# Optimization experiments

Hardware: AMD Instinct MI355X
Metric: run time of the kernel (lower is better)

Reference implementation:

```python
import jax, jax.numpy as jnp
import numpy as np

N_HEADS = 32
N_KV_HEADS = 8
HEAD_DIM = 64


def _apply_rope(x, cos, sin):
    # x: [b, s, h, d]; cos/sin: [s, d//2]; interleaved real/imag pairs
    xr = x[..., 0::2]
    xi = x[..., 1::2]
    c = cos[None, :, None, :]
    s = sin[None, :, None, :]
    out_r = xr * c - xi * s
    out_i = xr * s + xi * c
    return jnp.stack([out_r, out_i], axis=-1).reshape(x.shape)


def setup_inputs() -> dict:
    key = jax.random.key(0)
    ks = jax.random.split(key, 10)
    b, s, dim = 2, 512, 2048
    cache_len = 1536
    half = HEAD_DIM // 2
    pos = jnp.arange(cache_len, cache_len + s, dtype=jnp.float32)
    inv_freq = 1.0 / (10000.0 ** (jnp.arange(0, half, dtype=jnp.float32) / half))
    ang = pos[:, None] * inv_freq[None, :]
    scale = 0.02
    return {
        "x": jax.random.normal(ks[0], (b, s, dim), jnp.float32),
        "freqs_cos": jnp.cos(ang),
        "freqs_sin": jnp.sin(ang),
        "k_cache": jax.random.normal(ks[1], (b, N_KV_HEADS, cache_len, HEAD_DIM), jnp.float32),
        "v_cache": jax.random.normal(ks[2], (b, N_KV_HEADS, cache_len, HEAD_DIM), jnp.float32),
        "attn_mask": jnp.zeros((s, cache_len + s), jnp.float32),
        "wq": jax.random.normal(ks[3], (N_HEADS * HEAD_DIM, dim), jnp.float32) * scale,
        "wk": jax.random.normal(ks[4], (N_KV_HEADS * HEAD_DIM, dim), jnp.float32) * scale,
        "wv": jax.random.normal(ks[5], (N_KV_HEADS * HEAD_DIM, dim), jnp.float32) * scale,
        "wo": jax.random.normal(ks[6], (dim, N_HEADS * HEAD_DIM), jnp.float32) * scale,
    }


def reference(x, freqs_cos, freqs_sin, k_cache, v_cache, attn_mask, wq, wk, wv, wo):
    b, s, dim = x.shape
    n_rep = N_HEADS // N_KV_HEADS
    # QKV projections (nn.Linear: y = x @ W.T)
    q = (x @ wq.T).reshape(b, s, N_HEADS, HEAD_DIM)
    k = (x @ wk.T).reshape(b, s, N_KV_HEADS, HEAD_DIM)
    v = (x @ wv.T).reshape(b, s, N_KV_HEADS, HEAD_DIM)
    # RoPE on q, k
    q = _apply_rope(q, freqs_cos, freqs_sin)
    k = _apply_rope(k, freqs_cos, freqs_sin)
    # [b, h, s, d]
    q = q.transpose(0, 2, 1, 3)
    k = k.transpose(0, 2, 1, 3)
    v = v.transpose(0, 2, 1, 3)
    new_k, new_v = k, v
    # KV-cache concat along sequence dim
    k_full = jnp.concatenate([k_cache, k], axis=2)
    v_full = jnp.concatenate([v_cache, v], axis=2)
    # GQA: repeat_interleave kv heads
    if n_rep > 1:
        k_full = jnp.repeat(k_full, n_rep, axis=1)
        v_full = jnp.repeat(v_full, n_rep, axis=1)
    # SDPA
    scale = 1.0 / jnp.sqrt(jnp.asarray(HEAD_DIM, x.dtype))
    scores = jnp.einsum("bhqd,bhkd->bhqk", q, k_full) * scale + attn_mask
    probs = jax.nn.softmax(scores, axis=-1)
    out = jnp.einsum("bhqk,bhkd->bhqd", probs, v_full)
    out = out.transpose(0, 2, 1, 3).reshape(b, s, N_HEADS * HEAD_DIM)
    out = out @ wo.T
    return (out, new_k, new_v)
```

## Files before the change

### kernel.cpp

```cpp
#include <hip/hip_runtime.h>
#include <hip/hip_bf16.h>

typedef __attribute__((ext_vector_type(8))) short bf16x8;
typedef __attribute__((ext_vector_type(4))) float f32x4;
typedef unsigned short u16;

#define MFMA16(a, b, c) __builtin_amdgcn_mfma_f32_16x16x32_bf16(a, b, c, 0, 0, 0)
#define GLL(srcp, dstp) __builtin_amdgcn_global_load_lds(                      \
    (const __attribute__((address_space(1))) void*)(srcp),                     \
    (__attribute__((address_space(3))) void*)(dstp), 16, 0, 0)

__device__ __forceinline__ u16 f2b(float f) {
  union { float f; unsigned u; } a; a.f = f;
  return (u16)((a.u + 0x7FFFu + ((a.u >> 16) & 1u)) >> 16);
}
__device__ __forceinline__ unsigned pk2(float lo, float hi) {
  __hip_bfloat162 h = __float22bfloat162_rn(make_float2(lo, hi));
  return *reinterpret_cast<unsigned*>(&h);
}

__global__ __launch_bounds__(256) void prep(const float* __restrict__ x,
                                            const float* __restrict__ kc,
                                            u16* __restrict__ xb,
                                            u16* __restrict__ kfull) {
  const int c = blockIdx.x * 256 + threadIdx.x;
  const float* src;
  u16* dst;
  if (c < 524288) {
    src = x + (size_t)c * 4; dst = xb + (size_t)c * 4;
  } else {
    int l = c - 524288;
    int bh = l / 24576, r = l - bh * 24576;
    src = kc + (size_t)bh * 98304 + (size_t)r * 4;
    dst = kfull + (size_t)bh * 131072 + (size_t)r * 4;
  }
  const float4 v = *(const float4*)src;
  ushort4 o;
  o.x = f2b(v.x); o.y = f2b(v.y); o.z = f2b(v.z); o.w = f2b(v.w);
  *(ushort4*)dst = o;
}

__global__ __launch_bounds__(256) void vtr(const float* __restrict__ vc,
                                           const float* __restrict__ newv,
                                           u16* __restrict__ vT) {
  __shared__ float tile[64][65];
  const int kt = blockIdx.x, bh = blockIdx.y;
  const float* src;
  int colbase;
  if (kt < 24) {
    src = vc + ((size_t)bh * 1536 + (size_t)kt * 64) * 64;
    colbase = kt * 64;
  } else {
    src = newv + ((size_t)bh * 512 + (size_t)(kt - 24) * 64) * 64;
    colbase = 1536 + (kt - 24) * 64;
  }
  const int t = threadIdx.x;
#pragma unroll
  for (int j = 0; j < 4; j++) {
    int e = t + j * 256;
    int r = e >> 4, c = (e & 15) * 4;
    float4 v = *(const float4*)(src + (size_t)r * 64 + c);
    tile[r][c] = v.x; tile[r][c + 1] = v.y; tile[r][c + 2] = v.z; tile[r][c + 3] = v.w;
  }
  __syncthreads();
  int d = t >> 2, kv0 = (t & 3) * 16;
  u16* dst = vT + ((size_t)bh * 64 + d) * 2048 + colbase + kv0;
#pragma unroll
  for (int i = 0; i < 16; i++) dst[i] = f2b(tile[kv0 + i][d]);
}

__global__ __launch_bounds__(256, 3) void gemm_bt(const u16* __restrict__ A,
                                                  const float* __restrict__ B0,
                                                  const float* __restrict__ B1,
                                                  const float* __restrict__ B2,
                                                  float* __restrict__ Cp,
                                                  int M, int N, int K, int nb1, int nb2) {
  __shared__ __attribute__((aligned(16))) u16 As[2][4096];
  __shared__ __attribute__((aligned(16))) u16 Bs[2][8192];
  const int t = threadIdx.x;
  const int lane = t & 63, w = t >> 6;
  const int wr = (w >> 1) * 32, wc = (w & 1) * 64;
  const int g = lane >> 4, cc = lane & 15;
  const int nby = N >> 7, cpx = nby >> 3, nrt = M >> 6;
  const int j = blockIdx.x & 7, q = blockIdx.x >> 3;
  const int ct = j * cpx + (q % cpx);
  const int rest = q / cpx;
  const int rt = rest % nrt, ks = rest / nrt;
  const size_t row0 = (size_t)rt * 64;
  const int col0 = ct * 128;
  const int k0base = ks * (K >> 1);

  const int lr = lane >> 3, lc = lane & 7;
  const int swz = lc ^ lr;
  const u16* aS = A + (row0 + w * 16 + lr) * (size_t)K + swz * 8 + k0base;
  const float* Bb;
  int brow;
  if (col0 < nb1) { Bb = B0; brow = col0; }
  else if (col0 < nb2) { Bb = B1; brow = col0 - nb1; }
  else { Bb = B2; brow = col0 - nb2; }
  const float* bS = Bb + (brow + w * 32 + lr) * (size_t)K + swz * 8 + k0base;

  f32x4 acc[2][4] = {};
  f32x4 bl[4][2];

#define ALOAD(bufi, kk0)                                                       \
  {                                                                            \
    _Pragma("unroll") for (int i = 0; i < 2; i++)                              \
        GLL(aS + (size_t)(i * 8) * K + (kk0), &As[bufi][(w * 16 + i * 8) * 64]); \
  }
#define BLOAD(kk0)                                                             \
  {                                                                            \
    _Pragma("unroll") for (int i = 0; i < 4; i++) {                            \
      bl[i][0] = *(const f32x4*)(bS + (size_t)(i * 8) * K + (kk0));            \
      bl[i][1] = *(const f32x4*)(bS + (size_t)(i * 8) * K + (kk0) + 4);        \
    }                                                                          \
  }
#define BWRITE(bufi)                                                           \
  {                                                                            \
    _Pragma("unroll") for (int i = 0; i < 4; i++) {                            \
      uint4 pw;                                                                \
      pw.x = pk2(bl[i][0][0], bl[i][0][1]);                                    \
      pw.y = pk2(bl[i][0][2], bl[i][0][3]);                                    \
      pw.z = pk2(bl[i][1][0], bl[i][1][1]);                                    \
      pw.w = pk2(bl[i][1][2], bl[i][1][3]);                                    \
      *(uint4*)&Bs[bufi][(w * 32 + i * 8 + lr) * 64 + lc * 8] = pw;            \
    }                                                                          \
  }

  const int niter = (K >> 1) >> 6;
  BLOAD(0);
  ALOAD(0, 0);
  BWRITE(0);
  __syncthreads();

  for (int it = 0; it < niter; ++it) {
    const int buf = it & 1;
    if (it + 1 < niter) {
      BLOAD((it + 1) * 64);
      ALOAD(buf ^ 1, (it + 1) * 64);
    }
    bf16x8 av[2][2], bv[4][2];
#pragma unroll
    for (int m = 0; m < 2; m++) {
      const int row = wr + m * 16 + cc;
#pragma unroll
      for (int kk = 0; kk < 2; kk++)
        av[m][kk] = *(const bf16x8*)(&As[buf][row * 64 + (((kk * 4 + g) ^ (cc & 7)) * 8)]);
    }
#pragma unroll
    for (int n = 0; n < 4; n++) {
      const int row = wc + n * 16 + cc;
#pragma unroll
      for (int kk = 0; kk < 2; kk++)
        bv[n][kk] = *(const bf16x8*)(&Bs[buf][row * 64 + (((kk * 4 + g) ^ (cc & 7)) * 8)]);
    }
#pragma unroll
    for (int kk = 0; kk < 2; kk++)
#pragma unroll
      for (int m = 0; m < 2; m++)
#pragma unroll
        for (int n = 0; n < 4; n++)
          acc[m][n] = MFMA16(av[m][kk], bv[n][kk], acc[m][n]);
    if (it + 1 < niter) BWRITE(buf ^ 1);
    __syncthreads();
  }
#undef ALOAD
#undef BLOAD
#undef BWRITE
  float* Cw = Cp + (size_t)ks * M * N;
#pragma unroll
  for (int m = 0; m < 2; m++)
#pragma unroll
    for (int n = 0; n < 4; n++)
#pragma unroll
      for (int r = 0; r < 4; r++)
        Cw[(row0 + wr + m * 16 + g * 4 + r) * N + (col0 + wc + n * 16 + cc)] = acc[m][n][r];
}

__global__ __launch_bounds__(256) void postproc(const float* __restrict__ Cp0,
                                                const float* __restrict__ Cp1,
                                                const float* __restrict__ fcos,
                                                const float* __restrict__ fsin,
                                                u16* __restrict__ qrope,
                                                u16* __restrict__ kfull,
                                                float* __restrict__ newk,
                                                float* __restrict__ newv) {
  int idx = blockIdx.x * 256 + threadIdx.x;
  if (idx >= 1024 * 1536) return;
  int m = idx / 1536, p = idx - m * 1536;
  int b = m >> 9, s = m & 511;
  const float* r0 = Cp0 + (size_t)m * 3072;
  const float* r1 = Cp1 + (size_t)m * 3072;
  if (p < 1280) {
    bool isq = p < 1024;
    int pk = isq ? p : p - 1024;
    int h = pk >> 5, i = pk & 31;
    int colbase = (isq ? 0 : 2048) + h * 64 + 2 * i;
    float xr = r0[colbase] + r1[colbase];
    float xi = r0[colbase + 1] + r1[colbase + 1];
    float co = fcos[s * 32 + i], si = fsin[s * 32 + i];
    float orr = xr * co - xi * si;
    float oii = xr * si + xi * co;
    if (isq) {
      u16* dst = qrope + (((size_t)(b * 32 + h) * 512 + s) * 64 + 2 * i);
      dst[0] = f2b(orr); dst[1] = f2b(oii);
    } else {
      size_t o0 = ((size_t)(b * 8 + h) * 512 + s) * 64 + 2 * i;
      newk[o0] = orr; newk[o0 + 1] = oii;
      u16* kf = kfull + (((size_t)(b * 8 + h) * 2048 + 1536 + s) * 64 + 2 * i);
      kf[0] = f2b(orr); kf[1] = f2b(oii);
    }
  } else {
    int pv = p - 1280;
    int h = pv >> 5, i = pv & 31;
    int cb = 2560 + h * 64 + 2 * i;
    float v0 = r0[cb] + r1[cb], v1 = r0[cb + 1] + r1[cb + 1];
    size_t o0 = ((size_t)(b * 8 + h) * 512 + s) * 64 + 2 * i;
    newv[o0] = v0; newv[o0 + 1] = v1;
  }
}

__global__ __launch_bounds__(256) void sumout(const float* __restrict__ a,
                                              const float* __restrict__ b,
                                              float* __restrict__ out) {
  const int i = blockIdx.x * 256 + threadIdx.x;
  const float4 va = *(const float4*)(a + (size_t)i * 4);
  const float4 vb = *(const float4*)(b + (size_t)i * 4);
  float4 o;
  o.x = va.x + vb.x; o.y = va.y + vb.y; o.z = va.z + vb.z; o.w = va.w + vb.w;
  *(float4*)(out + (size_t)i * 4) = o;
}

__global__ __launch_bounds__(512, 4) void attn_split(const u16* __restrict__ qrope,
                                                     const u16* __restrict__ kfull,
                                                     const u16* __restrict__ vT,
                                                     const float* __restrict__ mask,
                                                     float* __restrict__ po,
                                                     float* __restrict__ ml) {
  __shared__ __attribute__((aligned(16))) u16 Ks[4][4096];
  __shared__ __attribute__((aligned(16))) u16 Vs[4][4096];
  __shared__ __attribute__((aligned(16))) u16 P_lds[8192];
  const int t = threadIdx.x, lane = t & 63, w = t >> 6;
  const int g = lane >> 4, cc = lane & 15;
  const int p = blockIdx.x;
  const int v = (p & 7) * 64 + (p >> 3);
  const int bh = v >> 3, qt = (v >> 1) & 3, sp = v & 1;
  const int b = bh >> 5, h = bh & 31;
  const int bhkv = b * 8 + (h >> 2);
  const int s0 = qt * 128 + w * 16;
  const int j0beg = sp * 1024;

  const int lr = lane >> 3, lc = lane & 7;
  const int swzc = lc ^ lr;

  bf16x8 qa0, qa1;
  {
    const u16* qb = qrope + ((size_t)bh * 512 + s0 + cc) * 64 + g * 8;
    qa0 = *(const bf16x8*)qb;
    qa1 = *(const bf16x8*)(qb + 32);
  }
  float mrow[4], lsum[4];
  f32x4 o[4] = {};
#pragma unroll
  for (int r = 0; r < 4; r++) { mrow[r] = -1e30f; lsum[r] = 0.0f; }

  u16* Pw = P_lds + w * 1024;
  const float* mbase = mask + (size_t)(s0 + g * 4) * 2048 + cc;
  const u16* ksrc0 = kfull + (size_t)bhkv * 131072 + (size_t)(w * 8 + lr) * 64 + swzc * 8;
  const u16* vsrc0 = vT + ((size_t)bhkv * 64 + w * 8 + lr) * 2048 + swzc * 8;

#pragma unroll
  for (int pt = 0; pt < 3; ++pt) {
    GLL(ksrc0 + (size_t)(j0beg + pt * 64) * 64, &Ks[pt][w * 512]);
    GLL(vsrc0 + (j0beg + pt * 64), &Vs[pt][w * 512]);
  }

  for (int it = 0; it < 16; ++it) {
    const int buf = it & 3;
    const int j0 = j0beg + it * 64;
    if (it < 14) {
      asm volatile("s_waitcnt vmcnt(4)" ::: "memory");
    } else if (it == 14) {
      asm volatile("s_waitcnt vmcnt(2)" ::: "memory");
    } else {
      asm volatile("s_waitcnt vmcnt(0)" ::: "memory");
    }
    __builtin_amdgcn_s_barrier();

    float mk[4][4];
#pragma unroll
    for (int r = 0; r < 4; r++)
#pragma unroll
      for (int jb = 0; jb < 4; jb++)
        mk[r][jb] = mbase[(size_t)r * 2048 + j0 + jb * 16];
    __builtin_amdgcn_sched_barrier(0);
    if (it < 13) {
      GLL(ksrc0 + (size_t)(j0 + 192) * 64, &Ks[(it + 3) & 3][w * 512]);
      GLL(vsrc0 + (j0 + 192), &Vs[(it + 3) & 3][w * 512]);
    }

    f32x4 sc[4];
    __builtin_amdgcn_s_setprio(1);
#pragma unroll
    for (int jb = 0; jb < 4; jb++) {
      const bf16x8 k0 = *(const bf16x8*)(&Ks[buf][(jb * 16 + cc) * 64 + ((g ^ (cc & 7)) * 8)]);
      const bf16x8 k1 =
          *(const bf16x8*)(&Ks[buf][(jb * 16 + cc) * 64 + (((g + 4) ^ (cc & 7)) * 8)]);
      f32x4 z = {0.f, 0.f, 0.f, 0.f};
      z = MFMA16(qa0, k0, z);
      z = MFMA16(qa1, k1, z);
      sc[jb] = z;
    }
    __builtin_amdgcn_s_setprio(0);
    float pp[4][4];
#pragma unroll
    for (int r = 0; r < 4; r++) {
#pragma unroll
      for (int jb = 0; jb < 4; jb++)
        pp[r][jb] = sc[jb][r] * 0.125f + mk[r][jb];
      const float lm = fmaxf(fmaxf(pp[r][0], pp[r][1]), fmaxf(pp[r][2], pp[r][3]));
      if (__any(lm > mrow[r] + 8.0f)) {
        float tm = lm;
#pragma unroll
        for (int off = 1; off < 16; off <<= 1) tm = fmaxf(tm, __shfl_xor(tm, off, 64));
        const float newm = fmaxf(mrow[r], tm);
        const float corr = __expf(mrow[r] - newm);
        mrow[r] = newm;
        lsum[r] *= corr;
#pragma unroll
        for (int db = 0; db < 4; db++) o[db][r] *= corr;
      }
      float ps = 0.f;
#pragma unroll
      for (int jb = 0; jb < 4; jb++) { pp[r][jb] = __expf(pp[r][jb] - mrow[r]); ps += pp[r][jb]; }
      lsum[r] += ps;
      const int rowb = (g * 4 + r) * 128;
      const int sw = ((g * 4 + r) & 7) << 4;
#pragma unroll
      for (int jb = 0; jb < 4; jb++)
        Pw[((rowb + (jb * 16 + cc) * 2) ^ sw) >> 1] = f2b(pp[r][jb]);
    }
    __builtin_amdgcn_s_setprio(1);
#pragma unroll
    for (int kk = 0; kk < 2; kk++) {
      const bf16x8 pa =
          *(const bf16x8*)(Pw + (((cc * 128 + kk * 64 + g * 16) ^ ((cc & 7) << 4)) >> 1));
#pragma unroll
      for (int db = 0; db < 4; db++) {
        const bf16x8 vf =
            *(const bf16x8*)(&Vs[buf][(db * 16 + cc) * 64 + (((kk * 4 + g) ^ (cc & 7)) * 8)]);
        o[db] = MFMA16(pa, vf, o[db]);
      }
    }
    __builtin_amdgcn_s_setprio(0);
  }
#pragma unroll
  for (int r = 0; r < 4; r++) {
    float ps = lsum[r];
#pragma unroll
    for (int off = 1; off < 16; off <<= 1) ps += __shfl_xor(ps, off, 64);
    const size_t row = (size_t)bh * 512 + s0 + g * 4 + r;
    float* dst = po + (row * 2 + sp) * 64 + cc;
#pragma unroll
    for (int db = 0; db < 4; db++) dst[db * 16] = o[db][r];
    if (cc == 0) {
      float2* mlp = (float2*)ml;
      mlp[row * 2 + sp] = make_float2(mrow[r], ps);
    }
  }
}

__global__ __launch_bounds__(256) void attn_combine(const float* __restrict__ po,
                                                    const float* __restrict__ ml,
                                                    u16* __restrict__ aout) {
  const int t = threadIdx.x;
  const int row = blockIdx.x * 4 + (t >> 6);
  const int d = t & 63;
  const int bh = row >> 9, s = row & 511;
  const int b = bh >> 5, h = bh & 31;
  const float2* mlp = (const float2*)ml;
  const float2 m0 = mlp[row * 2 + 0], m1 = mlp[row * 2 + 1];
  const float M = fmaxf(m0.x, m1.x);
  const float w0 = __expf(m0.x - M), w1 = __expf(m1.x - M);
  const float L = m0.y * w0 + m1.y * w1;
  const float o = po[(size_t)(row * 2 + 0) * 64 + d] * w0 +
                  po[(size_t)(row * 2 + 1) * 64 + d] * w1;
  aout[((size_t)(b * 512 + s)) * 2048 + h * 64 + d] = f2b(o / L);
}

extern "C" void kernel_launch(void* const* d_in, const int* in_sizes, int n_in,
                              void* d_out, int out_size, void* d_ws, size_t ws_size,
                              hipStream_t stream) {
  (void)in_sizes; (void)n_in; (void)out_size; (void)ws_size;
  const float* x    = (const float*)d_in[0];
  const float* fcos = (const float*)d_in[1];
  const float* fsin = (const float*)d_in[2];
  const float* kc   = (const float*)d_in[3];
  const float* vc   = (const float*)d_in[4];
  const float* mask = (const float*)d_in[5];
  const float* wq   = (const float*)d_in[6];
  const float* wk   = (const float*)d_in[7];
  const float* wv   = (const float*)d_in[8];
  const float* wo   = (const float*)d_in[9];

  float* out_f = (float*)d_out;
  float* newk  = out_f + 2097152;
  float* newv  = out_f + 2621440;

  u16*   xb    = (u16*)d_ws;
  float* Cp    = (float*)(xb + 2097152);
  float* Cp1   = Cp + 3145728;
  u16*   qrope = (u16*)(Cp + 6291456);
  u16*   kfull = qrope + 2097152;
  u16*   vTf   = kfull + 2097152;
  u16*   aout  = vTf + 2097152;
  float* ml    = (float*)(aout + 2097152);
  float* po    = (float*)d_ws;
  float* Co    = (float*)d_ws;
  float* Co1   = Co + 2097152;

  prep<<<3584, 256, 0, stream>>>(x, kc, xb, kfull);

  gemm_bt<<<768, 256, 0, stream>>>(xb, wq, wk, wv, Cp,
                                   1024, 3072, 2048, 2048, 2560);
  postproc<<<6144, 256, 0, stream>>>(Cp, Cp1, fcos, fsin, qrope, kfull, newk, newv);
  vtr<<<dim3(32, 16), 256, 0, stream>>>(vc, newv, vTf);
  attn_split<<<512, 512, 0, stream>>>(qrope, kfull, vTf, mask, po, ml);
  attn_combine<<<8192, 256, 0, stream>>>(po, ml, aout);
  gemm_bt<<<512, 256, 0, stream>>>(aout, wo, wo, wo, Co,
                                   1024, 2048, 2048, 4096, 8192);
  sumout<<<2048, 256, 0, stream>>>(Co, Co1, out_f);
}
```

Measured before the change: 124.5 us.

## Prefetch B tiles two iterations ahead with manual waitcnt barriers in GEMM

Restructures the split-K GEMM main loop so the fp32 B tile is loaded two iterations ahead into alternating register sets, while A keeps its one-ahead global_load_lds double buffering. The loop is unrolled by two, and __syncthreads is replaced by explicit s_waitcnt vmcnt/lgkmcnt plus s_barrier, so outstanding B loads can stay in flight across the barrier. The goal is to hide global load latency for B behind more MFMA work. In exchange it uses more VGPRs, which may lower occupancy. The hand-tuned vmcnt count also assumes a fixed number of loads and that niter is even.

Result: no change. 124.2 us (-0.2%).

```diff
diff --git a/kernel.cpp b/kernel.cpp
--- a/kernel.cpp
+++ b/kernel.cpp
@@ -101,72 +101,84 @@
   const float* bS = Bb + (brow + w * 32 + lr) * (size_t)K + swz * 8 + k0base;
 
   f32x4 acc[2][4] = {};
-  f32x4 bl[4][2];
+  f32x4 blA[4][2], blB[4][2];
 
 #define ALOAD(bufi, kk0)                                                       \
   {                                                                            \
     _Pragma("unroll") for (int i = 0; i < 2; i++)                              \
         GLL(aS + (size_t)(i * 8) * K + (kk0), &As[bufi][(w * 16 + i * 8) * 64]); \
   }
-#define BLOAD(kk0)                                                             \
+#define BLOAD(blv, kk0)                                                        \
   {                                                                            \
     _Pragma("unroll") for (int i = 0; i < 4; i++) {                            \
-      bl[i][0] = *(const f32x4*)(bS + (size_t)(i * 8) * K + (kk0));            \
-      bl[i][1] = *(const f32x4*)(bS + (size_t)(i * 8) * K + (kk0) + 4);        \
+      blv[i][0] = *(const f32x4*)(bS + (size_t)(i * 8) * K + (kk0));           \
+      blv[i][1] = *(const f32x4*)(bS + (size_t)(i * 8) * K + (kk0) + 4);       \
     }                                                                          \
   }
-#define BWRITE(bufi)                                                           \
+#define BWRITE(blv, bufi)                                                      \
   {                                                                            \
     _Pragma("unroll") for (int i = 0; i < 4; i++) {                            \
       uint4 pw;                                                                \
-      pw.x = pk2(bl[i][0][0], bl[i][0][1]);                                    \
-      pw.y = pk2(bl[i][0][2], bl[i][0][3]);                                    \
-      pw.z = pk2(bl[i][1][0], bl[i][1][1]);                                    \
-      pw.w = pk2(bl[i][1][2], bl[i][1][3]);                                    \
+      pw.x = pk2(blv[i][0][0], blv[i][0][1]);                                  \
+      pw.y = pk2(blv[i][0][2], blv[i][0][3]);                                  \
+      pw.z = pk2(blv[i][1][0], blv[i][1][1]);                                  \
+      pw.w = pk2(blv[i][1][2], blv[i][1][3]);                                  \
       *(uint4*)&Bs[bufi][(w * 32 + i * 8 + lr) * 64 + lc * 8] = pw;            \
     }                                                                          \
   }
 
   const int niter = (K >> 1) >> 6;
-  BLOAD(0);
+
   ALOAD(0, 0);
-  BWRITE(0);
-  __syncthreads();
-
-  for (int it = 0; it < niter; ++it) {
-    const int buf = it & 1;
-    if (it + 1 < niter) {
-      BLOAD((it + 1) * 64);
-      ALOAD(buf ^ 1, (it + 1) * 64);
-    }
-    bf16x8 av[2][2], bv[4][2];
-#pragma unroll
-    for (int m = 0; m < 2; m++) {
-      const int row = wr + m * 16 + cc;
-#pragma unroll
-      for (int kk = 0; kk < 2; kk++)
-        av[m][kk] = *(const bf16x8*)(&As[buf][row * 64 + (((kk * 4 + g) ^ (cc & 7)) * 8)]);
-    }
-#pragma unroll
-    for (int n = 0; n < 4; n++) {
-      const int row = wc + n * 16 + cc;
-#pragma unroll
-      for (int kk = 0; kk < 2; kk++)
-        bv[n][kk] = *(const bf16x8*)(&Bs[buf][row * 64 + (((kk * 4 + g) ^ (cc & 7)) * 8)]);
-    }
-#pragma unroll
-    for (int kk = 0; kk < 2; kk++)
-#pragma unroll
-      for (int m = 0; m < 2; m++)
-#pragma unroll
-        for (int n = 0; n < 4; n++)
-          acc[m][n] = MFMA16(av[m][kk], bv[n][kk], acc[m][n]);
-    if (it + 1 < niter) BWRITE(buf ^ 1);
-    __syncthreads();
-  }
+  BLOAD(blA, 0);
+  BWRITE(blA, 0);
+  BLOAD(blB, 64);
+  asm volatile("s_waitcnt lgkmcnt(0)" ::: "memory");
+  __builtin_amdgcn_s_barrier();
+
+#define GBODY(it_, blPrev, blCur)                                              \
+  {                                                                            \
+    const int buf = (it_) & 1;                                                 \
+    if ((it_) > 0) {                                                           \
+      if ((it_) + 1 < niter) {                                                 \
+        asm volatile("s_waitcnt vmcnt(8)" ::: "memory");                       \
+      } else {                                                                 \
+        asm volatile("s_waitcnt vmcnt(0)" ::: "memory");                       \
+      }                                                                        \
+      asm volatile("s_waitcnt lgkmcnt(0)" ::: "memory");                       \
+      __builtin_amdgcn_s_barrier();                                            \
+    }                                                                          \
+    if ((it_) + 1 < niter) ALOAD(buf ^ 1, ((it_) + 1) * 64);                   \
+    if ((it_) + 2 < niter) BLOAD(blCur, ((it_) + 2) * 64);                     \
+    bf16x8 av[2][2], bv[4][2];                                                 \
+    _Pragma("unroll") for (int m = 0; m < 2; m++) {                            \
+      const int row = wr + m * 16 + cc;                                        \
+      _Pragma("unroll") for (int kk = 0; kk < 2; kk++)                         \
+          av[m][kk] =                                                          \
+              *(const bf16x8*)(&As[buf][row * 64 + (((kk * 4 + g) ^ (cc & 7)) * 8)]); \
+    }                                                                          \
+    _Pragma("unroll") for (int n = 0; n < 4; n++) {                            \
+      const int row = wc + n * 16 + cc;                                        \
+      _Pragma("unroll") for (int kk = 0; kk < 2; kk++)                         \
+          bv[n][kk] =                                                          \
+              *(const bf16x8*)(&Bs[buf][row * 64 + (((kk * 4 + g) ^ (cc & 7)) * 8)]); \
+    }                                                                          \
+    _Pragma("unroll") for (int kk = 0; kk < 2; kk++)                           \
+        _Pragma("unroll") for (int m = 0; m < 2; m++)                          \
+        _Pragma("unroll") for (int n = 0; n < 4; n++)                          \
+            acc[m][n] = MFMA16(av[m][kk], bv[n][kk], acc[m][n]);               \
+    if ((it_) + 1 < niter) BWRITE(blPrev, buf ^ 1);                            \
+  }
+
+  for (int it = 0; it < niter; it += 2) {
+    GBODY(it, blB, blA);
+    GBODY(it + 1, blA, blB);
+  }
+#undef GBODY
 #undef ALOAD
 #undef BLOAD
 #undef BWRITE
+
   float* Cw = Cp + (size_t)ks * M * N;
 #pragma unroll
   for (int m = 0; m < 2; m++)
```
